# Kernel optimization log

Measured on AMD Instinct MI355X. Metric: run time of the kernel, lower is better.

The kernel has to match this reference:

```python
import jax, jax.numpy as jnp
import numpy as np

N_NODES = 100000
N_EDGES = 1600000
IN_CH = 128
HID = 64
N_CLASSES = 16
N_GRAPHS = 64


def setup_inputs() -> dict:
    key = jax.random.key(0)
    ks = jax.random.split(key, 10)
    x = jax.random.normal(ks[0], (N_NODES, IN_CH), dtype=jnp.float32)
    edge_index = jax.random.randint(ks[1], (2, N_EDGES), 0, N_NODES, dtype=jnp.int64)
    edge_weight = jax.random.uniform(ks[2], (N_EDGES,), dtype=jnp.float32)
    batch = jnp.sort(jax.random.randint(ks[3], (N_NODES,), 0, N_GRAPHS, dtype=jnp.int64))
    s1 = 1.0 / np.sqrt(IN_CH)
    s2 = 1.0 / np.sqrt(HID)
    W1 = jax.random.uniform(ks[4], (IN_CH, HID), jnp.float32, -s1, s1)
    b1 = jnp.zeros((HID,), jnp.float32)
    W2 = jax.random.uniform(ks[5], (HID, HID), jnp.float32, -s2, s2)
    b2 = jnp.zeros((HID,), jnp.float32)
    Wl = jax.random.uniform(ks[6], (HID, N_CLASSES), jnp.float32, -s2, s2)
    bl = jax.random.uniform(ks[7], (N_CLASSES,), jnp.float32, -s2, s2)
    return {"x": x, "edge_index": edge_index, "edge_weight": edge_weight,
            "batch": batch, "W1": W1, "b1": b1, "W2": W2, "b2": b2,
            "Wl": Wl, "bl": bl}


def _gcn_conv(x, src, dst, ew, W, b, n_nodes):
    # PyG GCNConv: h = x @ W; symmetric normalization with self-loops;
    # out[dst] += norm * h[src]; out += bias.
    deg = jax.ops.segment_sum(ew, dst, num_segments=n_nodes)
    deg_inv_sqrt = jnp.where(deg > 0, jax.lax.rsqrt(jnp.maximum(deg, 1e-30)), 0.0)
    norm = deg_inv_sqrt[src] * ew * deg_inv_sqrt[dst]  # [E']
    h = x @ W                                          # [N, out]
    msg = h[src] * norm[:, None]                       # [E', out] gather
    out = jax.ops.segment_sum(msg, dst, num_segments=n_nodes)  # scatter-add
    return out + b


def reference(x, edge_index, edge_weight, batch, W1, b1, W2, b2, Wl, bl):
    n = x.shape[0]
    # add self loops once (weight 1.0), shared by both conv layers
    loop = jnp.arange(n, dtype=edge_index.dtype)
    src = jnp.concatenate([edge_index[0], loop])
    dst = jnp.concatenate([edge_index[1], loop])
    ew = jnp.concatenate([edge_weight, jnp.ones((n,), edge_weight.dtype)])

    h = jax.nn.relu(_gcn_conv(x, src, dst, ew, W1, b1, n))
    h = jax.nn.relu(_gcn_conv(h, src, dst, ew, W2, b2, n))

    # global_mean_pool over graphs
    sums = jax.ops.segment_sum(h, batch, num_segments=N_GRAPHS)  # [G, HID]
    cnt = jax.ops.segment_sum(jnp.ones((n,), h.dtype), batch, num_segments=N_GRAPHS)
    pooled = sums / jnp.maximum(cnt, 1.0)[:, None]

    return pooled @ Wl + bl
```

## Files before the change

### kernel.cpp

```cpp
#include <hip/hip_runtime.h>
#include <hip/hip_fp16.h>

#define N_NODES   100000
#define N_EDGES   1600000
#define IN_CH     128
#define HID       64
#define N_CLASSES 16
#define N_GRAPHS  64

#define BK_SH     9
#define BK_NODES  512
#define NB        ((N_NODES + BK_NODES - 1) / BK_NODES)
#define BK_CAP    10240
#define CH_EDGES  4096
#define EPT       16
#define NCH       ((N_EDGES + CH_EDGES - 1) / CH_EDGES)
#define AGG_NPW   8

typedef __attribute__((ext_vector_type(8))) short bf16x8;
typedef __attribute__((ext_vector_type(4))) float f32x4;

__device__ __forceinline__ unsigned short f2bf(float f) {
    unsigned u = __float_as_uint(f);
    u += 0x7fffu + ((u >> 16) & 1u);
    return (unsigned short)(u >> 16);
}
__device__ __forceinline__ float4 bf4(uint2 v) {
    float4 o;
    o.x = __uint_as_float(v.x << 16);
    o.y = __uint_as_float(v.x & 0xffff0000u);
    o.z = __uint_as_float(v.y << 16);
    o.w = __uint_as_float(v.y & 0xffff0000u);
    return o;
}
__device__ __forceinline__ float dec_ew(unsigned v) {
    return __half2float(__ushort_as_half((unsigned short)(v >> 17)));
}

__global__ void k_init(int* __restrict__ bcursor, float* __restrict__ pooled,
                       float* __restrict__ cnt) {
    int i = blockIdx.x * 256 + threadIdx.x;
    if (i < NB) bcursor[i] = i * BK_CAP;
    if (i < N_GRAPHS * HID) pooled[i] = 0.0f;
    if (i < N_GRAPHS) cnt[i] = 0.0f;
}

__global__ void k_binscatter(const int* __restrict__ src, const int* __restrict__ dst,
                             const float* __restrict__ ew, int* __restrict__ bcursor,
                             int2* __restrict__ bedges) {
    __shared__ int  hist[NB];
    __shared__ int  offs[NB];
    __shared__ int  gbase[NB];
    __shared__ int  sc[256];
    __shared__ int2 stage[CH_EDGES];
    __shared__ int  dest[CH_EDGES];
    const int t = threadIdx.x;
    const int base = blockIdx.x * CH_EDGES;
    const int nloc = min(CH_EDGES, N_EDGES - base);

    for (int i = t; i < NB; i += 256) hist[i] = 0;
    __syncthreads();

    int myb[EPT], myr[EPT], myp[EPT]; float myw[EPT];
#pragma unroll
    for (int j = 0; j < EPT; ++j) {
        int i = base + j * 256 + t;
        if (i < N_EDGES) {
            int s = src[i], d = dst[i];
            int b = d >> BK_SH;
            myb[j] = b;
            myr[j] = atomicAdd(&hist[b], 1);
            myp[j] = s | ((d & (BK_NODES - 1)) << 17);
            myw[j] = ew[i];
        } else {
            myb[j] = -1;
        }
    }
    __syncthreads();

    int v = (t < NB) ? hist[t] : 0;
    sc[t] = v;
    __syncthreads();
    for (int off = 1; off < 256; off <<= 1) {
        int a = (t >= off) ? sc[t - off] : 0;
        __syncthreads();
        sc[t] += a;
        __syncthreads();
    }
    if (t < NB) {
        offs[t] = sc[t] - v;
        gbase[t] = (v > 0) ? atomicAdd(&bcursor[t], v) : 0;
    }
    __syncthreads();

#pragma unroll
    for (int j = 0; j < EPT; ++j) {
        if (myb[j] >= 0) {
            int p = offs[myb[j]] + myr[j];
            stage[p] = make_int2(myp[j], __float_as_int(myw[j]));
            dest[p] = gbase[myb[j]] + myr[j];
        }
    }
    __syncthreads();

    for (int i = t; i < nloc; i += 256)
        bedges[dest[i]] = stage[i];
}

__global__ __launch_bounds__(256) void k_build(const int* __restrict__ bcursor,
                                               const int2* __restrict__ bedges,
                                               int2* __restrict__ rowse,
                                               float* __restrict__ dis,
                                               unsigned* __restrict__ csr) {
    __shared__ int2  eds[BK_CAP];
    __shared__ int   cnt[BK_NODES];
    __shared__ float dsum[BK_NODES];
    __shared__ int   cur[BK_NODES];
    __shared__ int   sc[256];
    const int b = blockIdx.x;
    const int t = threadIdx.x;
    const int beg = b * BK_CAP, end = bcursor[b];
    const int n = end - beg;

    for (int i = t; i < BK_NODES; i += 256) { cnt[i] = 0; dsum[i] = 0.0f; }
    __syncthreads();

    for (int i = t; i < n; i += 256) {
        int2 e = bedges[beg + i];
        eds[i] = e;
        int dl = ((unsigned)e.x) >> 17;
        atomicAdd(&cnt[dl], 1);
        atomicAdd(&dsum[dl], __int_as_float(e.y));
    }
    __syncthreads();

    int a0 = cnt[2 * t], a1 = cnt[2 * t + 1];
    int pair = a0 + a1;
    sc[t] = pair;
    __syncthreads();
    for (int off = 1; off < 256; off <<= 1) {
        int a = (t >= off) ? sc[t - off] : 0;
        __syncthreads();
        sc[t] += a;
        __syncthreads();
    }
    int excl = sc[t] - pair;
    cur[2 * t] = excl;
    cur[2 * t + 1] = excl + a0;
    {
        int n0 = b * BK_NODES + 2 * t;
        if (n0 < N_NODES) {
            rowse[n0] = make_int2(beg + excl, beg + excl + a0);
            dis[n0] = rsqrtf(1.0f + dsum[2 * t]);
        }
        int n1 = n0 + 1;
        if (n1 < N_NODES) {
            rowse[n1] = make_int2(beg + excl + a0, beg + excl + a0 + a1);
            dis[n1] = rsqrtf(1.0f + dsum[2 * t + 1]);
        }
    }
    __syncthreads();

    for (int i = t; i < n; i += 256) {
        int2 e = eds[i];
        int dl = ((unsigned)e.x) >> 17;
        int s = e.x & 0x1FFFF;
        unsigned short w16 = __half_as_ushort(__float2half(__int_as_float(e.y)));
        int pos = beg + atomicAdd(&cur[dl], 1);
        csr[pos] = (unsigned)s | ((unsigned)w16 << 17);
    }
}

template <int K>
__global__ __launch_bounds__(256) void k_gemm(const float* __restrict__ x,
                                              const float* __restrict__ W,
                                              const float* __restrict__ dis,
                                              unsigned short* __restrict__ hb) {
    constexpr int AS = K + 8;
    __shared__ unsigned short a_s[64 * AS];
    __shared__ unsigned short wt[64 * AS];
    const int t    = threadIdx.x;
    const int lane = t & 63;
    const int wave = t >> 6;
    const int m    = lane & 15;
    const int quad = lane >> 4;
    const int rowbase = blockIdx.x * 64;

    constexpr int CPR = K / 8;
    for (int c = t; c < 64 * CPR; c += 256) {
        int row = c / CPR, cc = c % CPR;
        int gr = rowbase + row;
        float4 v0, v1;
        if (gr < N_NODES) {
            v0 = *(const float4*)&x[(long)gr * K + cc * 8];
            v1 = *(const float4*)&x[(long)gr * K + cc * 8 + 4];
        } else {
            v0 = make_float4(0.f, 0.f, 0.f, 0.f); v1 = v0;
        }
        uint4 p;
        p.x = f2bf(v0.x) | ((unsigned)f2bf(v0.y) << 16);
        p.y = f2bf(v0.z) | ((unsigned)f2bf(v0.w) << 16);
        p.z = f2bf(v1.x) | ((unsigned)f2bf(v1.y) << 16);
        p.w = f2bf(v1.z) | ((unsigned)f2bf(v1.w) << 16);
        *(uint4*)&a_s[row * AS + cc * 8] = p;
    }
    for (int idx = t; idx < K * 64; idx += 256) {
        int k = idx >> 6, n = idx & 63;
        wt[n * AS + k] = f2bf(W[idx]);
    }
    __syncthreads();

    bf16x8 bfrag[4][K / 32];
#pragma unroll
    for (int nt = 0; nt < 4; ++nt)
#pragma unroll
        for (int ks = 0; ks < K / 32; ++ks)
            bfrag[nt][ks] = *(const bf16x8*)&wt[(nt * 16 + m) * AS + ks * 32 + quad * 8];

    f32x4 acc[4];
#pragma unroll
    for (int nt = 0; nt < 4; ++nt) acc[nt] = (f32x4){0.f, 0.f, 0.f, 0.f};

#pragma unroll
    for (int ks = 0; ks < K / 32; ++ks) {
        bf16x8 af = *(const bf16x8*)&a_s[(wave * 16 + m) * AS + ks * 32 + quad * 8];
#pragma unroll
        for (int nt = 0; nt < 4; ++nt)
            acc[nt] = __builtin_amdgcn_mfma_f32_16x16x32_bf16(af, bfrag[nt][ks],
                                                              acc[nt], 0, 0, 0);
    }

#pragma unroll
    for (int i = 0; i < 4; ++i) {
        int gr = rowbase + wave * 16 + quad * 4 + i;
        if (gr < N_NODES) {
            float dsc = dis[gr];
#pragma unroll
            for (int nt = 0; nt < 4; ++nt)
                hb[(long)gr * HID + nt * 16 + m] = f2bf(dsc * acc[nt][i]);
        }
    }
}

__global__ void k_aggregate(const int2* __restrict__ rowse, const unsigned* __restrict__ csr,
                            const uint2* __restrict__ hb, const float* __restrict__ dis,
                            const float* __restrict__ b, float4* __restrict__ out4) {
    const int tid  = threadIdx.x;
    const int lane = tid & 63;
    const int g    = lane >> 4;
    const int c4   = lane & 15;
    const int nodebase = (blockIdx.x * 4 + (tid >> 6)) * AGG_NPW;
    const float4 bb = ((const float4*)b)[c4];

    if (nodebase >= N_NODES) return;

    int2 rs = rowse[nodebase];
    uint2 hsr = hb[nodebase * 16 + c4];

    for (int j = 0; j < AGG_NPW; ++j) {
        const int node = nodebase + j;
        if (node >= N_NODES) return;

        const int2 rs_c = rs;
        const float4 hs = bf4(hsr);
        if (j + 1 < AGG_NPW && node + 1 < N_NODES) {
            rs  = rowse[node + 1];
            hsr = hb[(node + 1) * 16 + c4];
        }

        float4 acc;
        if (g == 0) { acc = hs; }
        else        { acc.x = 0.f; acc.y = 0.f; acc.z = 0.f; acc.w = 0.f; }

        int p = rs_c.x;
        const int end = rs_c.y;

        unsigned d0, d1, d2, d3;
        if (p + 16 <= end) {
            d0 = csr[p + g];     d1 = csr[p + 4 + g];
            d2 = csr[p + 8 + g]; d3 = csr[p + 12 + g];
        }
        while (p + 16 <= end) {
            const unsigned e0 = d0, e1 = d1, e2 = d2, e3 = d3;
            const int pn = p + 16;
            if (pn + 16 <= end) {
                d0 = csr[pn + g];     d1 = csr[pn + 4 + g];
                d2 = csr[pn + 8 + g]; d3 = csr[pn + 12 + g];
            }
            float4 v0 = bf4(hb[(e0 & 0x1FFFF) * 16 + c4]);
            float4 v1 = bf4(hb[(e1 & 0x1FFFF) * 16 + c4]);
            float4 v2 = bf4(hb[(e2 & 0x1FFFF) * 16 + c4]);
            float4 v3 = bf4(hb[(e3 & 0x1FFFF) * 16 + c4]);
            float w0 = dec_ew(e0), w1 = dec_ew(e1);
            float w2 = dec_ew(e2), w3 = dec_ew(e3);
            acc.x += w0 * v0.x; acc.y += w0 * v0.y; acc.z += w0 * v0.z; acc.w += w0 * v0.w;
            acc.x += w1 * v1.x; acc.y += w1 * v1.y; acc.z += w1 * v1.z; acc.w += w1 * v1.w;
            acc.x += w2 * v2.x; acc.y += w2 * v2.y; acc.z += w2 * v2.z; acc.w += w2 * v2.w;
            acc.x += w3 * v3.x; acc.y += w3 * v3.y; acc.z += w3 * v3.z; acc.w += w3 * v3.w;
            p = pn;
        }
        if (p < end) {
            int i0 = p + g, i1 = p + 4 + g, i2 = p + 8 + g, i3 = p + 12 + g;
            unsigned e0 = csr[min(i0, end - 1)];
            unsigned e1 = csr[min(i1, end - 1)];
            unsigned e2 = csr[min(i2, end - 1)];
            unsigned e3 = csr[min(i3, end - 1)];
            float4 v0 = bf4(hb[(e0 & 0x1FFFF) * 16 + c4]);
            float4 v1 = bf4(hb[(e1 & 0x1FFFF) * 16 + c4]);
            float4 v2 = bf4(hb[(e2 & 0x1FFFF) * 16 + c4]);
            float4 v3 = bf4(hb[(e3 & 0x1FFFF) * 16 + c4]);
            float w0 = (i0 < end) ? dec_ew(e0) : 0.0f;
            float w1 = (i1 < end) ? dec_ew(e1) : 0.0f;
            float w2 = (i2 < end) ? dec_ew(e2) : 0.0f;
            float w3 = (i3 < end) ? dec_ew(e3) : 0.0f;
            acc.x += w0 * v0.x; acc.y += w0 * v0.y; acc.z += w0 * v0.z; acc.w += w0 * v0.w;
            acc.x += w1 * v1.x; acc.y += w1 * v1.y; acc.z += w1 * v1.z; acc.w += w1 * v1.w;
            acc.x += w2 * v2.x; acc.y += w2 * v2.y; acc.z += w2 * v2.z; acc.w += w2 * v2.w;
            acc.x += w3 * v3.x; acc.y += w3 * v3.y; acc.z += w3 * v3.z; acc.w += w3 * v3.w;
        }

        acc.x += __shfl_xor(acc.x, 16); acc.y += __shfl_xor(acc.y, 16);
        acc.z += __shfl_xor(acc.z, 16); acc.w += __shfl_xor(acc.w, 16);
        acc.x += __shfl_xor(acc.x, 32); acc.y += __shfl_xor(acc.y, 32);
        acc.z += __shfl_xor(acc.z, 32); acc.w += __shfl_xor(acc.w, 32);

        if (g == 0) {
            const float dd = dis[node];
            float4 o;
            o.x = fmaxf(dd * acc.x + bb.x, 0.0f);
            o.y = fmaxf(dd * acc.y + bb.y, 0.0f);
            o.z = fmaxf(dd * acc.z + bb.z, 0.0f);
            o.w = fmaxf(dd * acc.w + bb.w, 0.0f);
            out4[node * 16 + c4] = o;
        }
    }
}

#define POOL_NPB 256
__global__ __launch_bounds__(1024) void k_pool(const float* __restrict__ agg,
                                               const int* __restrict__ batch,
                                               float* __restrict__ pooled,
                                               float* __restrict__ cnt) {
    __shared__ float psh[N_GRAPHS * HID];
    __shared__ float csh[N_GRAPHS];
    const int tid = threadIdx.x;
    const int c = tid & 63;
    const int w = tid >> 6;
    const int nodebase = blockIdx.x * POOL_NPB + w * 16;

    for (int i = tid; i < N_GRAPHS * HID; i += 1024) psh[i] = 0.f;
    if (tid < N_GRAPHS) csh[tid] = 0.f;
    __syncthreads();

    int curg = -1; float accv = 0.f, cntacc = 0.f;
    for (int j = 0; j < 16; ++j) {
        int node = nodebase + j;
        if (node >= N_NODES) break;
        int g = batch[node];
        float v = agg[node * HID + c];
        if (g != curg) {
            if (curg >= 0) {
                atomicAdd(&psh[curg * HID + c], accv);
                if (c == 0) atomicAdd(&csh[curg], cntacc);
            }
            curg = g; accv = 0.f; cntacc = 0.f;
        }
        accv += v; cntacc += 1.f;
    }
    if (curg >= 0) {
        atomicAdd(&psh[curg * HID + c], accv);
        if (c == 0) atomicAdd(&csh[curg], cntacc);
    }
    __syncthreads();

    for (int i = tid; i < N_GRAPHS * HID; i += 1024) {
        if (csh[i >> 6] > 0.f) atomicAdd(&pooled[i], psh[i]);
    }
    if (tid < N_GRAPHS && csh[tid] > 0.f) atomicAdd(&cnt[tid], csh[tid]);
}

__global__ void k_out(const float* __restrict__ pooled, const float* __restrict__ cnt,
                      const float* __restrict__ Wl, const float* __restrict__ bl,
                      float* __restrict__ out) {
    int tid = threadIdx.x;
    int g = tid >> 4, k = tid & 15;
    float inv = 1.0f / fmaxf(cnt[g], 1.0f);
    float acc = 0.f;
#pragma unroll
    for (int h = 0; h < HID; ++h) acc += pooled[g * HID + h] * Wl[h * N_CLASSES + k];
    out[g * N_CLASSES + k] = acc * inv + bl[k];
}

extern "C" void kernel_launch(void* const* d_in, const int* in_sizes, int n_in,
                              void* d_out, int out_size, void* d_ws, size_t ws_size,
                              hipStream_t stream) {
    const float* x     = (const float*)d_in[0];
    const int*   ei    = (const int*)d_in[1];
    const float* ew    = (const float*)d_in[2];
    const int*   batch = (const int*)d_in[3];
    const float* W1    = (const float*)d_in[4];
    const float* b1    = (const float*)d_in[5];
    const float* W2    = (const float*)d_in[6];
    const float* b2    = (const float*)d_in[7];
    const float* Wl    = (const float*)d_in[8];
    const float* bl    = (const float*)d_in[9];

    const int* srcv = ei;
    const int* dstv = ei + N_EDGES;

    char* wsb = (char*)d_ws;
    float*          dis    = (float*)wsb;              wsb += 100352 * 4;
    int2*           rowse  = (int2*)wsb;               wsb += 100352 * 8;
    int*            bcursor= (int*)wsb;                wsb += 256 * 4;
    unsigned*       csr    = (unsigned*)wsb;           wsb += (size_t)NB * BK_CAP * 4;
    unsigned short* hb     = (unsigned short*)wsb;     wsb += N_NODES * HID * 2;
    float*          agg    = (float*)wsb;              wsb += N_NODES * HID * 4;
    float*          pooled = (float*)wsb;              wsb += N_GRAPHS * HID * 4;
    float*          cnt    = (float*)wsb;              wsb += N_GRAPHS * 4;
    float*          out    = (float*)d_out;
    int2*           bedges = (int2*)agg;

    k_init<<<16, 256, 0, stream>>>(bcursor, pooled, cnt);
    k_binscatter<<<NCH, 256, 0, stream>>>(srcv, dstv, ew, bcursor, bedges);
    k_build<<<NB, 256, 0, stream>>>(bcursor, bedges, rowse, dis, csr);

    const int agg_blocks = (N_NODES + 4 * AGG_NPW - 1) / (4 * AGG_NPW);

    k_gemm<IN_CH><<<(N_NODES + 63) / 64, 256, 0, stream>>>(x, W1, dis, hb);
    k_aggregate<<<agg_blocks, 256, 0, stream>>>(rowse, csr, (const uint2*)hb,
                                                dis, b1, (float4*)agg);
    k_gemm<HID><<<(N_NODES + 63) / 64, 256, 0, stream>>>(agg, W2, dis, hb);
    k_aggregate<<<agg_blocks, 256, 0, stream>>>(rowse, csr, (const uint2*)hb,
                                                dis, b2, (float4*)agg);

    k_pool<<<(N_NODES + POOL_NPB - 1) / POOL_NPB, 1024, 0, stream>>>(
        agg, batch, pooled, cnt);
    k_out<<<1, N_GRAPHS * N_CLASSES, 0, stream>>>(pooled, cnt, Wl, bl, out);
}
```

Measured before the change: 271.1 us.

## Store layer-1 output as bf16, use buffer loads in aggregate, shrink nodes per wave

The first aggregation now writes its ReLU output as packed bf16 instead of fp32. The second GEMM then reads MFMA A-fragments straight from global memory, with no LDS staging or conversion. The aggregation gathers use raw buffer loads with 32-bit offsets and vector float math, and nodes per wave drop from 8 to 2 so more waves run in parallel. This cuts intermediate memory traffic and address arithmetic, at the cost of one more bf16 rounding step on the layer-1 activations.

```diff
diff --git a/kernel.cpp b/kernel.cpp
--- a/kernel.cpp
+++ b/kernel.cpp
@@ -15,27 +15,57 @@
 #define CH_EDGES  4096
 #define EPT       16
 #define NCH       ((N_EDGES + CH_EDGES - 1) / CH_EDGES)
-#define AGG_NPW   8
+#define AGG_NPW   2
 
 typedef __attribute__((ext_vector_type(8))) short bf16x8;
 typedef __attribute__((ext_vector_type(4))) float f32x4;
+typedef __attribute__((ext_vector_type(4))) unsigned u32x4;
+typedef __attribute__((ext_vector_type(2))) unsigned u32x2;
 
 __device__ __forceinline__ unsigned short f2bf(float f) {
     unsigned u = __float_as_uint(f);
     u += 0x7fffu + ((u >> 16) & 1u);
     return (unsigned short)(u >> 16);
 }
-__device__ __forceinline__ float4 bf4(uint2 v) {
-    float4 o;
-    o.x = __uint_as_float(v.x << 16);
-    o.y = __uint_as_float(v.x & 0xffff0000u);
-    o.z = __uint_as_float(v.y << 16);
-    o.w = __uint_as_float(v.y & 0xffff0000u);
-    return o;
+__device__ __forceinline__ f32x4 bf4v(uint2 v) {
+    u32x4 u;
+    u.x = v.x << 16; u.y = v.x & 0xffff0000u;
+    u.z = v.y << 16; u.w = v.y & 0xffff0000u;
+    return __builtin_bit_cast(f32x4, u);
 }
 __device__ __forceinline__ float dec_ew(unsigned v) {
     return __half2float(__ushort_as_half((unsigned short)(v >> 17)));
 }
+
+#if __has_builtin(__builtin_amdgcn_make_buffer_rsrc) && \
+    __has_builtin(__builtin_amdgcn_raw_buffer_load_b32) && \
+    __has_builtin(__builtin_amdgcn_raw_buffer_load_b64)
+struct BufView {
+    __amdgpu_buffer_rsrc_t rsrc;
+    __device__ __forceinline__ void init(const void* p) {
+        rsrc = __builtin_amdgcn_make_buffer_rsrc((void*)p, (short)0,
+                                                 (int)0xFFFFFFFF, 0x00020000);
+    }
+    __device__ __forceinline__ unsigned ld32(unsigned off) const {
+        return __builtin_amdgcn_raw_buffer_load_b32(rsrc, (int)off, 0, 0);
+    }
+    __device__ __forceinline__ uint2 ld64(unsigned off) const {
+        u32x2 r = __builtin_amdgcn_raw_buffer_load_b64(rsrc, (int)off, 0, 0);
+        return make_uint2(r.x, r.y);
+    }
+};
+#else
+struct BufView {
+    const char* base;
+    __device__ __forceinline__ void init(const void* p) { base = (const char*)p; }
+    __device__ __forceinline__ unsigned ld32(unsigned off) const {
+        return *(const unsigned*)(base + off);
+    }
+    __device__ __forceinline__ uint2 ld64(unsigned off) const {
+        return *(const uint2*)(base + off);
+    }
+};
+#endif
 
 __global__ void k_init(int* __restrict__ bcursor, float* __restrict__ pooled,
                        float* __restrict__ cnt) {
@@ -171,13 +201,13 @@
     }
 }
 
-template <int K>
+template <int K, bool INB>
 __global__ __launch_bounds__(256) void k_gemm(const float* __restrict__ x,
+                                              const unsigned short* __restrict__ xb,
                                               const float* __restrict__ W,
                                               const float* __restrict__ dis,
                                               unsigned short* __restrict__ hb) {
     constexpr int AS = K + 8;
-    __shared__ unsigned short a_s[64 * AS];
     __shared__ unsigned short wt[64 * AS];
     const int t    = threadIdx.x;
     const int lane = t & 63;
@@ -186,29 +216,51 @@
     const int quad = lane >> 4;
     const int rowbase = blockIdx.x * 64;
 
-    constexpr int CPR = K / 8;
-    for (int c = t; c < 64 * CPR; c += 256) {
-        int row = c / CPR, cc = c % CPR;
-        int gr = rowbase + row;
-        float4 v0, v1;
-        if (gr < N_NODES) {
-            v0 = *(const float4*)&x[(long)gr * K + cc * 8];
-            v1 = *(const float4*)&x[(long)gr * K + cc * 8 + 4];
-        } else {
-            v0 = make_float4(0.f, 0.f, 0.f, 0.f); v1 = v0;
-        }
-        uint4 p;
-        p.x = f2bf(v0.x) | ((unsigned)f2bf(v0.y) << 16);
-        p.y = f2bf(v0.z) | ((unsigned)f2bf(v0.w) << 16);
-        p.z = f2bf(v1.x) | ((unsigned)f2bf(v1.y) << 16);
-        p.w = f2bf(v1.z) | ((unsigned)f2bf(v1.w) << 16);
-        *(uint4*)&a_s[row * AS + cc * 8] = p;
-    }
-    for (int idx = t; idx < K * 64; idx += 256) {
-        int k = idx >> 6, n = idx & 63;
-        wt[n * AS + k] = f2bf(W[idx]);
-    }
-    __syncthreads();
+    bf16x8 afrag[K / 32];
+
+    if constexpr (!INB) {
+        __shared__ unsigned short a_s[64 * AS];
+        constexpr int CPR = K / 8;
+        for (int c = t; c < 64 * CPR; c += 256) {
+            int row = c / CPR, cc = c % CPR;
+            int gr = rowbase + row;
+            float4 v0, v1;
+            if (gr < N_NODES) {
+                v0 = *(const float4*)&x[(long)gr * K + cc * 8];
+                v1 = *(const float4*)&x[(long)gr * K + cc * 8 + 4];
+            } else {
+                v0 = make_float4(0.f, 0.f, 0.f, 0.f); v1 = v0;
+            }
+            uint4 p;
+            p.x = f2bf(v0.x) | ((unsigned)f2bf(v0.y) << 16);
+            p.y = f2bf(v0.z) | ((unsigned)f2bf(v0.w) << 16);
+            p.z = f2bf(v1.x) | ((unsigned)f2bf(v1.y) << 16);
+            p.w = f2bf(v1.z) | ((unsigned)f2bf(v1.w) << 16);
+            *(uint4*)&a_s[row * AS + cc * 8] = p;
+        }
+        for (int idx = t; idx < K * 64; idx += 256) {
+            int k = idx >> 6, n = idx & 63;
+            wt[n * AS + k] = f2bf(W[idx]);
+        }
+        __syncthreads();
+#pragma unroll
+        for (int ks = 0; ks < K / 32; ++ks)
+            afrag[ks] = *(const bf16x8*)&a_s[(wave * 16 + m) * AS + ks * 32 + quad * 8];
+    } else {
+        const int gr = rowbase + wave * 16 + m;
+#pragma unroll
+        for (int ks = 0; ks < K / 32; ++ks) {
+            if (gr < N_NODES)
+                afrag[ks] = *(const bf16x8*)&xb[(long)gr * K + ks * 32 + quad * 8];
+            else
+                afrag[ks] = (bf16x8){0, 0, 0, 0, 0, 0, 0, 0};
+        }
+        for (int idx = t; idx < K * 64; idx += 256) {
+            int k = idx >> 6, n = idx & 63;
+            wt[n * AS + k] = f2bf(W[idx]);
+        }
+        __syncthreads();
+    }
 
     bf16x8 bfrag[4][K / 32];
 #pragma unroll
@@ -223,10 +275,9 @@
 
 #pragma unroll
     for (int ks = 0; ks < K / 32; ++ks) {
-        bf16x8 af = *(const bf16x8*)&a_s[(wave * 16 + m) * AS + ks * 32 + quad * 8];
 #pragma unroll
         for (int nt = 0; nt < 4; ++nt)
-            acc[nt] = __builtin_amdgcn_mfma_f32_16x16x32_bf16(af, bfrag[nt][ks],
+            acc[nt] = __builtin_amdgcn_mfma_f32_16x16x32_bf16(afrag[ks], bfrag[nt][ks],
                                                               acc[nt], 0, 0, 0);
     }
 
@@ -242,96 +293,108 @@
     }
 }
 
+template <bool OB>
 __global__ void k_aggregate(const int2* __restrict__ rowse, const unsigned* __restrict__ csr,
                             const uint2* __restrict__ hb, const float* __restrict__ dis,
-                            const float* __restrict__ b, float4* __restrict__ out4) {
+                            const float* __restrict__ b, float4* __restrict__ out4,
+                            uint2* __restrict__ outb) {
     const int tid  = threadIdx.x;
     const int lane = tid & 63;
     const int g    = lane >> 4;
     const int c4   = lane & 15;
     const int nodebase = (blockIdx.x * 4 + (tid >> 6)) * AGG_NPW;
     const float4 bb = ((const float4*)b)[c4];
+    const f32x4 bbv = {bb.x, bb.y, bb.z, bb.w};
 
     if (nodebase >= N_NODES) return;
+
+    BufView vc; vc.init(csr);
+    BufView vh; vh.init(hb);
+    const unsigned coff = (unsigned)(c4 << 3);
 
     int2 rs = rowse[nodebase];
     uint2 hsr = hb[nodebase * 16 + c4];
 
     for (int j = 0; j < AGG_NPW; ++j) {
         const int node = nodebase + j;
-        if (node >= N_NODES) return;
-
         const int2 rs_c = rs;
-        const float4 hs = bf4(hsr);
-        if (j + 1 < AGG_NPW && node + 1 < N_NODES) {
+        const f32x4 hsv = bf4v(hsr);
+        if (j + 1 < AGG_NPW) {
             rs  = rowse[node + 1];
             hsr = hb[(node + 1) * 16 + c4];
         }
 
-        float4 acc;
-        if (g == 0) { acc = hs; }
-        else        { acc.x = 0.f; acc.y = 0.f; acc.z = 0.f; acc.w = 0.f; }
+        f32x4 acc = (g == 0) ? hsv : (f32x4){0.f, 0.f, 0.f, 0.f};
 
         int p = rs_c.x;
         const int end = rs_c.y;
 
         unsigned d0, d1, d2, d3;
         if (p + 16 <= end) {
-            d0 = csr[p + g];     d1 = csr[p + 4 + g];
-            d2 = csr[p + 8 + g]; d3 = csr[p + 12 + g];
+            const unsigned v = (unsigned)((p + g) << 2);
+            d0 = vc.ld32(v);      d1 = vc.ld32(v + 16);
+            d2 = vc.ld32(v + 32); d3 = vc.ld32(v + 48);
         }
         while (p + 16 <= end) {
             const unsigned e0 = d0, e1 = d1, e2 = d2, e3 = d3;
             const int pn = p + 16;
             if (pn + 16 <= end) {
-                d0 = csr[pn + g];     d1 = csr[pn + 4 + g];
-                d2 = csr[pn + 8 + g]; d3 = csr[pn + 12 + g];
+                const unsigned v = (unsigned)((pn + g) << 2);
+                d0 = vc.ld32(v);      d1 = vc.ld32(v + 16);
+                d2 = vc.ld32(v + 32); d3 = vc.ld32(v + 48);
             }
-            float4 v0 = bf4(hb[(e0 & 0x1FFFF) * 16 + c4]);
-            float4 v1 = bf4(hb[(e1 & 0x1FFFF) * 16 + c4]);
-            float4 v2 = bf4(hb[(e2 & 0x1FFFF) * 16 + c4]);
-            float4 v3 = bf4(hb[(e3 & 0x1FFFF) * 16 + c4]);
-            float w0 = dec_ew(e0), w1 = dec_ew(e1);
-            float w2 = dec_ew(e2), w3 = dec_ew(e3);
-            acc.x += w0 * v0.x; acc.y += w0 * v0.y; acc.z += w0 * v0.z; acc.w += w0 * v0.w;
-            acc.x += w1 * v1.x; acc.y += w1 * v1.y; acc.z += w1 * v1.z; acc.w += w1 * v1.w;
-            acc.x += w2 * v2.x; acc.y += w2 * v2.y; acc.z += w2 * v2.z; acc.w += w2 * v2.w;
-            acc.x += w3 * v3.x; acc.y += w3 * v3.y; acc.z += w3 * v3.z; acc.w += w3 * v3.w;
+            f32x4 v0 = bf4v(vh.ld64(((e0 & 0x1FFFF) << 7) | coff));
+            f32x4 v1 = bf4v(vh.ld64(((e1 & 0x1FFFF) << 7) | coff));
+            f32x4 v2 = bf4v(vh.ld64(((e2 & 0x1FFFF) << 7) | coff));
+            f32x4 v3 = bf4v(vh.ld64(((e3 & 0x1FFFF) << 7) | coff));
+            acc += v0 * dec_ew(e0);
+            acc += v1 * dec_ew(e1);
+            acc += v2 * dec_ew(e2);
+            acc += v3 * dec_ew(e3);
             p = pn;
         }
         if (p < end) {
-            int i0 = p + g, i1 = p + 4 + g, i2 = p + 8 + g, i3 = p + 12 + g;
-            unsigned e0 = csr[min(i0, end - 1)];
-            unsigned e1 = csr[min(i1, end - 1)];
-            unsigned e2 = csr[min(i2, end - 1)];
-            unsigned e3 = csr[min(i3, end - 1)];
-            float4 v0 = bf4(hb[(e0 & 0x1FFFF) * 16 + c4]);
-            float4 v1 = bf4(hb[(e1 & 0x1FFFF) * 16 + c4]);
-            float4 v2 = bf4(hb[(e2 & 0x1FFFF) * 16 + c4]);
-            float4 v3 = bf4(hb[(e3 & 0x1FFFF) * 16 + c4]);
-            float w0 = (i0 < end) ? dec_ew(e0) : 0.0f;
-            float w1 = (i1 < end) ? dec_ew(e1) : 0.0f;
-            float w2 = (i2 < end) ? dec_ew(e2) : 0.0f;
-            float w3 = (i3 < end) ? dec_ew(e3) : 0.0f;
-            acc.x += w0 * v0.x; acc.y += w0 * v0.y; acc.z += w0 * v0.z; acc.w += w0 * v0.w;
-            acc.x += w1 * v1.x; acc.y += w1 * v1.y; acc.z += w1 * v1.z; acc.w += w1 * v1.w;
-            acc.x += w2 * v2.x; acc.y += w2 * v2.y; acc.z += w2 * v2.z; acc.w += w2 * v2.w;
-            acc.x += w3 * v3.x; acc.y += w3 * v3.y; acc.z += w3 * v3.z; acc.w += w3 * v3.w;
-        }
-
-        acc.x += __shfl_xor(acc.x, 16); acc.y += __shfl_xor(acc.y, 16);
-        acc.z += __shfl_xor(acc.z, 16); acc.w += __shfl_xor(acc.w, 16);
-        acc.x += __shfl_xor(acc.x, 32); acc.y += __shfl_xor(acc.y, 32);
-        acc.z += __shfl_xor(acc.z, 32); acc.w += __shfl_xor(acc.w, 32);
+            const int i0 = p + g, i1 = p + 4 + g, i2 = p + 8 + g, i3 = p + 12 + g;
+            const int last = end - 1;
+            unsigned e0 = vc.ld32((unsigned)(min(i0, last) << 2));
+            unsigned e1 = vc.ld32((unsigned)(min(i1, last) << 2));
+            unsigned e2 = vc.ld32((unsigned)(min(i2, last) << 2));
+            unsigned e3 = vc.ld32((unsigned)(min(i3, last) << 2));
+            f32x4 v0 = bf4v(vh.ld64(((e0 & 0x1FFFF) << 7) | coff));
+            f32x4 v1 = bf4v(vh.ld64(((e1 & 0x1FFFF) << 7) | coff));
+            f32x4 v2 = bf4v(vh.ld64(((e2 & 0x1FFFF) << 7) | coff));
+            f32x4 v3 = bf4v(vh.ld64(((e3 & 0x1FFFF) << 7) | coff));
+            const float w0 = (i0 < end) ? dec_ew(e0) : 0.0f;
+            const float w1 = (i1 < end) ? dec_ew(e1) : 0.0f;
+            const float w2 = (i2 < end) ? dec_ew(e2) : 0.0f;
+            const float w3 = (i3 < end) ? dec_ew(e3) : 0.0f;
+            acc += v0 * w0;
+            acc += v1 * w1;
+            acc += v2 * w2;
+            acc += v3 * w3;
+        }
+
+#pragma unroll
+        for (int i = 0; i < 4; ++i) {
+            float ta = acc[i];
+            ta += __shfl_xor(ta, 16);
+            ta += __shfl_xor(ta, 32);
+            acc[i] = ta;
+        }
 
         if (g == 0) {
             const float dd = dis[node];
-            float4 o;
-            o.x = fmaxf(dd * acc.x + bb.x, 0.0f);
-            o.y = fmaxf(dd * acc.y + bb.y, 0.0f);
-            o.z = fmaxf(dd * acc.z + bb.z, 0.0f);
-            o.w = fmaxf(dd * acc.w + bb.w, 0.0f);
-            out4[node * 16 + c4] = o;
+            f32x4 o = acc * dd + bbv;
+            o.x = fmaxf(o.x, 0.0f); o.y = fmaxf(o.y, 0.0f);
+            o.z = fmaxf(o.z, 0.0f); o.w = fmaxf(o.w, 0.0f);
+            if constexpr (OB) {
+                uint2 pk;
+                pk.x = (unsigned)f2bf(o.x) | ((unsigned)f2bf(o.y) << 16);
+                pk.y = (unsigned)f2bf(o.z) | ((unsigned)f2bf(o.w) << 16);
+                outb[node * 16 + c4] = pk;
+            } else {
+                *(f32x4*)&out4[node * 16 + c4] = o;
+            }
         }
     }
 }
@@ -419,6 +482,7 @@
     float*          cnt    = (float*)wsb;              wsb += N_GRAPHS * 4;
     float*          out    = (float*)d_out;
     int2*           bedges = (int2*)agg;
+    unsigned short* hbA    = (unsigned short*)agg;
 
     k_init<<<16, 256, 0, stream>>>(bcursor, pooled, cnt);
     k_binscatter<<<NCH, 256, 0, stream>>>(srcv, dstv, ew, bcursor, bedges);
@@ -426,12 +490,12 @@
 
     const int agg_blocks = (N_NODES + 4 * AGG_NPW - 1) / (4 * AGG_NPW);
 
-    k_gemm<IN_CH><<<(N_NODES + 63) / 64, 256, 0, stream>>>(x, W1, dis, hb);
-    k_aggregate<<<agg_blocks, 256, 0, stream>>>(rowse, csr, (const uint2*)hb,
-                                                dis, b1, (float4*)agg);
-    k_gemm<HID><<<(N_NODES + 63) / 64, 256, 0, stream>>>(agg, W2, dis, hb);
-    k_aggregate<<<agg_blocks, 256, 0, stream>>>(rowse, csr, (const uint2*)hb,
-                                                dis, b2, (float4*)agg);
+    k_gemm<IN_CH, false><<<(N_NODES + 63) / 64, 256, 0, stream>>>(x, nullptr, W1, dis, hb);
+    k_aggregate<true><<<agg_blocks, 256, 0, stream>>>(rowse, csr, (const uint2*)hb,
+                                                      dis, b1, nullptr, (uint2*)hbA);
+    k_gemm<HID, true><<<(N_NODES + 63) / 64, 256, 0, stream>>>(nullptr, hbA, W2, dis, hb);
+    k_aggregate<false><<<agg_blocks, 256, 0, stream>>>(rowse, csr, (const uint2*)hb,
+                                                       dis, b2, (float4*)agg, nullptr);
 
     k_pool<<<(N_NODES + POOL_NPB - 1) / POOL_NPB, 1024, 0, stream>>>(
         agg, batch, pooled, cnt);
```

Result: faster. 260.3 us (-4.0%).
